# Performance work log

Measured on AMD Instinct MI355X. Metric: run time of the kernel, lower is better.

The kernel has to match this reference:

```python
import jax, jax.numpy as jnp
import numpy as np

B, S, H = 2, 2048, 2048
NUM_HEADS, HEAD_DIM = 16, 128
SOFTMAX_SHIFT = 12


def _int_project(x, w_i8, b_i32, out_shift):
    # x: [..., in] int32, w_i8: [in, out] int8, b_i32: [out] int32
    y = jnp.matmul(x.astype(jnp.int32), w_i8.astype(jnp.int32))
    y = y + b_i32
    return jnp.right_shift(y, out_shift)  # arithmetic shift on signed int32


def setup_inputs() -> dict:
    key = jax.random.key(0)
    ks = jax.random.split(key, 9)
    x_i32 = jax.random.randint(ks[0], (B, S, H), 0, 256, dtype=jnp.int32)
    def w(k):
        return jax.random.randint(k, (H, H), -127, 128, dtype=jnp.int32).astype(jnp.int8)
    def b(k):
        return jax.random.randint(k, (H,), -64, 64, dtype=jnp.int32)
    return {
        "x_i32": x_i32,
        "wq": w(ks[1]), "bq": b(ks[2]),
        "wk": w(ks[3]), "bk": b(ks[4]),
        "wv": w(ks[5]), "bv": b(ks[6]),
        "wo": w(ks[7]), "bo": b(ks[8]),
    }


def reference(x_i32, wq, bq, wk, bk, wv, bv, wo, bo):
    bsz, seq, hidden = x_i32.shape

    def heads(t):  # [b, s, h] -> [b, nh, s, hd]
        return t.reshape(bsz, seq, NUM_HEADS, HEAD_DIM).transpose(0, 2, 1, 3)

    q = heads(_int_project(x_i32, wq, bq, 6))
    k = heads(_int_project(x_i32, wk, bk, 6))
    v = heads(_int_project(x_i32, wv, bv, 6))

    # int32 scores [b, nh, s, s], halved by arithmetic right shift
    scores = jnp.right_shift(jnp.einsum("bhqd,bhkd->bhqk", q, k), 1)

    idx = jnp.arange(seq)
    causal = idx[:, None] >= idx[None, :]  # [s, s]
    neg = jnp.int32(-(1 << 20))
    masked = jnp.where(causal[None, None], scores, neg)

    # clamp-softmax surrogate: subtract row max, clamp(x + 256, 0, 2^12 - 1)
    shifted = masked - jnp.max(masked, axis=-1, keepdims=True)
    attn = jnp.clip(shifted + 256, 0, (1 << SOFTMAX_SHIFT) - 1)

    context = jnp.right_shift(jnp.einsum("bhqk,bhkd->bhqd", attn, v), SOFTMAX_SHIFT)
    context = context.transpose(0, 2, 1, 3).reshape(bsz, seq, hidden)
    return _int_project(context, wo, bo, 7)
```

## Files before the change

kernel.cpp:

```cpp
#include <hip/hip_runtime.h>
#include <stdint.h>


#define SEQ   2048
#define HID   2048
#define NHEAD 16
#define HDIM  128
#define NB    2
#define NEGV  (-(1 << 20))
#define PLANE 8388608
#define WSZ   4194304
#define BHSTR 262144

#define AS1 __attribute__((address_space(1)))
#define AS3 __attribute__((address_space(3)))

typedef int v4i __attribute__((ext_vector_type(4)));

__device__ __forceinline__ v4i mfma_i8(v4i a, v4i b, v4i c) {
  return __builtin_amdgcn_mfma_i32_16x16x64_i8(a, b, c, 0, 0, 0);
}

__device__ __forceinline__ void gl16(const char* g, char* l) {
  __builtin_amdgcn_global_load_lds((const AS1 uint32_t*)g, (AS3 uint32_t*)l, 16, 0, 0);
}

__device__ __forceinline__ void limb3(int v, int& l0, int& l1, int& l2) {
  l0 = (v << 24) >> 24;
  int t = (v - l0) >> 8;
  l1 = (t << 24) >> 24;
  l2 = (t - l1) >> 8;
}

__device__ __forceinline__ int sext4(int x) {
  return ((x << 24) >> 24) + ((x << 16) >> 24) + ((x << 8) >> 24) + (x >> 24);
}

__global__ __launch_bounds__(256) void xpack(const int* __restrict__ X, char* __restrict__ Xs8)
{
  const int i = blockIdx.x * 256 + threadIdx.x;
  int4 v = ((const int4*)X)[i];
  uint32_t b = (uint32_t)((v.x - 128) & 255)
             | ((uint32_t)((v.y - 128) & 255) << 8)
             | ((uint32_t)((v.z - 128) & 255) << 16)
             | ((uint32_t)((v.w - 128) & 255) << 24);
  ((uint32_t*)Xs8)[i] = b;
}

__global__ __launch_bounds__(256) void wpack(const int* __restrict__ Wq, const int* __restrict__ Wk,
                                             const int* __restrict__ Wv, const int* __restrict__ Wo,
                                             char* __restrict__ WtQKV, char* __restrict__ WtO)
{
  __shared__ char Ws[128 * 144];
  const int z = blockIdx.z;
  const int* W = (z == 0) ? Wq : (z == 1) ? Wk : (z == 2) ? Wv : Wo;
  char* Wt = (z < 3) ? (WtQKV + (size_t)z * WSZ) : WtO;
  const int k0 = blockIdx.x * 128, n0 = blockIdx.y * 128;
  const int t = threadIdx.x;
  const int lr = t >> 1, lc = (t & 1) * 64;
  const int* wp = W + (size_t)(k0 + lr) * HID + n0 + lc;
#pragma unroll
  for (int i = 0; i < 16; i++) {
    int4 v = *(const int4*)(wp + 4 * i);
    uint32_t pb = (uint32_t)(v.x & 255) | ((uint32_t)(v.y & 255) << 8)
                | ((uint32_t)(v.z & 255) << 16) | ((uint32_t)(v.w & 255) << 24);
    *(uint32_t*)&Ws[lr * 144 + lc + 4 * i] = pb;
  }
  __syncthreads();
  const int nl = t >> 1, kh = (t & 1) * 64;
  char* op = Wt + (size_t)(n0 + nl) * HID + k0 + kh;
#pragma unroll
  for (int w = 0; w < 16; w++) {
    uint32_t u = 0;
#pragma unroll
    for (int j = 0; j < 4; j++)
      u |= ((uint32_t)(unsigned char)Ws[(kh + w * 4 + j) * 144 + nl]) << (8 * j);
    *(uint32_t*)(op + 4 * w) = u;
  }
}

__global__ __launch_bounds__(256) void csum(const char* __restrict__ WtQKV,
                                            const int* __restrict__ Bq, const int* __restrict__ Bk,
                                            const int* __restrict__ Bv, int* __restrict__ bias2)
{
  const int id = blockIdx.x;
  const int z = id >> 9;
  const int n = ((id & 511) << 2) + (threadIdx.x >> 6);
  const int lane = threadIdx.x & 63;
  const int4* p = (const int4*)(WtQKV + (size_t)z * WSZ + (size_t)n * HID + lane * 32);
  int4 a = p[0], b4 = p[1];
  int vals[8] = {a.x, a.y, a.z, a.w, b4.x, b4.y, b4.z, b4.w};
  int s = 0;
#pragma unroll
  for (int i = 0; i < 8; i++) s += sext4(vals[i]);
#pragma unroll
  for (int m = 1; m < 64; m <<= 1) s += __shfl_xor(s, m);
  if (lane == 0) {
    const int* B = (z == 0) ? Bq : (z == 1) ? Bk : Bv;
    bias2[z * HID + n] = (int)((uint32_t)B[n] + ((uint32_t)s << 7));
  }
}

__global__ __launch_bounds__(256, 3) void qkv_mfma(const char* __restrict__ Xs8,
                                                   const char* __restrict__ WtQKV,
                                                   const int* __restrict__ bias2,
                                                   char* __restrict__ QL, char* __restrict__ KL,
                                                   int* __restrict__ VR, int* __restrict__ PS)
{
  __shared__ __align__(16) char smem[33792];
  const int id = blockIdx.x;
  const int n0 = (id & 15) * 128;
  const int zm = id >> 4;
  const int z  = zm >> 5;
  const int m0 = (zm & 31) * 128;
  const char* Wt = WtQKV + (size_t)z * WSZ;
  const int* b2 = bias2 + z * HID;

  const int t = threadIdx.x, wave = t >> 6, lane = t & 63;
  const int r16 = lane & 15, quad = lane >> 4;
  const int wm = (wave >> 1) * 64, wn = (wave & 1) * 64;

  const int lr0 = t >> 2;
  const int lc0 = (t & 3) ^ ((lr0 >> 1) & 3);
  const int lr1 = (t + 256) >> 2;
  const int lc1 = (t & 3) ^ ((lr1 >> 1) & 3);
  const char* Ag0 = Xs8 + (size_t)(m0 + lr0) * HID + lc0 * 16;
  const char* Ag1 = Xs8 + (size_t)(m0 + lr1) * HID + lc1 * 16;
  const char* Bg0 = Wt + (size_t)(n0 + lr0) * HID + lc0 * 16;
  const char* Bg1 = Wt + (size_t)(n0 + lr1) * HID + lc1 * 16;
  char* Al0 = smem + wave * 1024;
  char* Al1 = smem + 4096 + wave * 1024;
  char* Bl0 = smem + 8192 + wave * 1024;
  char* Bl1 = smem + 12288 + wave * 1024;

  const int xq = (quad ^ ((r16 >> 1) & 3)) * 16;

  v4i acc[4][4];
#pragma unroll
  for (int i = 0; i < 4; i++)
#pragma unroll
    for (int j = 0; j < 4; j++) acc[i][j] = (v4i){0, 0, 0, 0};

  for (int k0 = 0; k0 < HID; k0 += 64) {
    gl16(Ag0 + k0, Al0);
    gl16(Ag1 + k0, Al1);
    gl16(Bg0 + k0, Bl0);
    gl16(Bg1 + k0, Bl1);
    __syncthreads();
    v4i Af[4], Bf[4];
#pragma unroll
    for (int mt = 0; mt < 4; mt++)
      Af[mt] = *(const v4i*)(smem + (wm + mt * 16 + r16) * 64 + xq);
#pragma unroll
    for (int nt = 0; nt < 4; nt++)
      Bf[nt] = *(const v4i*)(smem + 8192 + (wn + nt * 16 + r16) * 64 + xq);
#pragma unroll
    for (int mt = 0; mt < 4; mt++)
#pragma unroll
      for (int nt = 0; nt < 4; nt++)
        acc[mt][nt] = mfma_i8(Af[mt], Bf[nt], acc[mt][nt]);
    __syncthreads();
  }

  int bvv[4];
#pragma unroll
  for (int nt = 0; nt < 4; nt++) bvv[nt] = b2[n0 + wn + nt * 16 + r16];

  const int h  = id & 15;
  const int b  = m0 >> 11;
  const int s0 = m0 & 2047;
  const int bh = b * 16 + h;
  const int myhalf = wave >> 1;

  if (z <= 1) {
    char* dplane = (z == 0) ? QL : KL;
#pragma unroll
    for (int half = 0; half < 2; half++) {
      __syncthreads();
      if (myhalf == half) {
#pragma unroll
        for (int mt = 0; mt < 4; mt++)
#pragma unroll
          for (int nt = 0; nt < 4; nt++) {
            const int col = wn + nt * 16 + r16;
#pragma unroll
            for (int r = 0; r < 4; r++) {
              const int y = ((int)((uint32_t)acc[mt][nt][r] + (uint32_t)bvv[nt])) >> 6;
              int l0, l1, l2; limb3(y, l0, l1, l2);
              const int off = (mt * 16 + quad * 4 + r) * 144 + col;
              smem[off]         = (char)l0;
              smem[9216 + off]  = (char)l1;
              smem[18432 + off] = (char)l2;
            }
          }
      }
      __syncthreads();
      if (t < 192) {
        const int l = t >> 6, rc = t & 63;
        const char* src = &smem[l * 9216 + rc * 144];
        char* dp = dplane + (size_t)l * PLANE + (size_t)bh * BHSTR
                 + (size_t)(s0 + half * 64 + rc) * 128;
#pragma unroll
        for (int j = 0; j < 8; j++)
          *(int4*)(dp + j * 16) = *(const int4*)(src + j * 16);
      }
    }
  } else {
    int* s32 = (int*)smem;
#pragma unroll
    for (int half = 0; half < 2; half++) {
      __syncthreads();
      if (myhalf == half) {
#pragma unroll
        for (int mt = 0; mt < 4; mt++)
#pragma unroll
          for (int nt = 0; nt < 4; nt++) {
            const int col = wn + nt * 16 + r16;
#pragma unroll
            for (int r = 0; r < 4; r++) {
              const int y = ((int)((uint32_t)acc[mt][nt][r] + (uint32_t)bvv[nt])) >> 6;
              s32[(mt * 16 + quad * 4 + r) * 132 + col] = y;
            }
          }
      }
      __syncthreads();
      {
        const int rr = t >> 2, cs = (t & 3) * 32;
        int* vp = VR + (size_t)bh * (SEQ * HDIM) + (size_t)(s0 + half * 64 + rr) * HDIM + cs;
        const int* sp = s32 + rr * 132 + cs;
#pragma unroll
        for (int j = 0; j < 8; j++)
          *(int4*)(vp + 4 * j) = *(const int4*)(sp + 4 * j);
      }
      if (t < 128) {
        uint32_t a = 0;
        for (int j = 0; j < 64; j++) a += (uint32_t)s32[j * 132 + t];
        PS[((size_t)bh * 32 + (s0 >> 6) + half) * 128 + t] = (int)a;
      }
    }
  }
}

__global__ __launch_bounds__(128) void suf(const int* __restrict__ PS, int* __restrict__ SUF)
{
  const int bh = blockIdx.x, d = threadIdx.x;
  SUF[((size_t)bh * 33 + 32) * 128 + d] = 0;
  uint32_t acc = 0;
  for (int tt = 31; tt >= 0; tt--) {
    acc += (uint32_t)PS[((size_t)bh * 32 + tt) * 128 + d];
    SUF[((size_t)bh * 33 + tt) * 128 + d] = (int)acc;
  }
}

__global__ __launch_bounds__(256, 4) void attn_mfma(const char* __restrict__ QL,
    const char* __restrict__ KL, const int* __restrict__ VR,
    const int* __restrict__ SUF, char* __restrict__ CL)
{
  __shared__ __align__(16) char smK[24576];
  __shared__ int   candS[32 * 32];
  __shared__ unsigned short candK[32 * 32];
  __shared__ int   mrow[32];
  __shared__ int   cnt[32];

  const int t = threadIdx.x, w = t >> 6, lane = t & 63;
  const int r16 = lane & 15, quad = lane >> 4;
  const int bid = blockIdx.x;
  const int bh = bid & 31;
  const int tile = 63 - (bid >> 5);
  const int q0 = tile * 32;
  const int b = bh >> 4, h = bh & 15;
  const char* QLb = QL + (size_t)bh * BHSTR;
  const char* KLb = KL + (size_t)bh * BHSTR;
  const int g = w >> 1, p = w & 1;
  const int wq = q0 + g * 16;
  const int ktlast = q0 >> 6;

  if (t < 32) { mrow[t] = (int)0x80000000; cnt[t] = 0; }

  const int srow = w * 8 + (lane >> 3);
  const int schunk = (lane & 7) ^ (lane >> 3);
  const char* kg0 = KLb + (size_t)srow * 128 + schunk * 16;
  const char* kg1 = KLb + (size_t)(srow + 32) * 128 + schunk * 16;

  v4i Aq[3][2];
  {
    const char* qb = QLb + (size_t)(wq + r16) * 128 + quad * 16;
#pragma unroll
    for (int l = 0; l < 3; l++)
#pragma unroll
      for (int c = 0; c < 2; c++)
        Aq[l][c] = *(const v4i*)(qb + (size_t)l * PLANE + c * 64);
  }

  int qrow[4], mr[4];
#pragma unroll
  for (int r = 0; r < 4; r++) {
    qrow[r] = wq + quad * 4 + r;
    mr[r] = (qrow[r] == SEQ - 1) ? (int)0x80000000 : NEGV;
  }
  __syncthreads();

  const v4i vzero = (v4i){0, 0, 0, 0};
  const int sw0 = (((0 * 4 + quad) ^ (r16 & 7))) * 16;
  const int sw1 = (((1 * 4 + quad) ^ (r16 & 7))) * 16;

  for (int kt = 0; kt <= ktlast; kt++) {
    const size_t kb = (size_t)kt * 8192;
#pragma unroll
    for (int l = 0; l < 3; l++) {
      gl16(kg0 + (size_t)l * PLANE + kb, smK + l * 8192 + w * 1024);
      gl16(kg1 + (size_t)l * PLANE + kb, smK + l * 8192 + 4096 + w * 1024);
    }
    __syncthreads();

    const bool last = (kt == ktlast);
    int sc[2][4];
#pragma unroll
    for (int nt2 = 0; nt2 < 2; nt2++) {
      const int nt = 2 * p + nt2;
      const char* kbase = smK + (nt * 16 + r16) * 128;
      v4i B[3][2];
#pragma unroll
      for (int l = 0; l < 3; l++) {
        B[l][0] = *(const v4i*)(kbase + l * 8192 + sw0);
        B[l][1] = *(const v4i*)(kbase + l * 8192 + sw1);
      }
      v4i c0, c1, c2, c3;
      c0 = mfma_i8(Aq[0][0], B[0][0], vzero);
      c0 = mfma_i8(Aq[0][1], B[0][1], c0);
      c1 = mfma_i8(Aq[0][0], B[1][0], vzero);
      c1 = mfma_i8(Aq[0][1], B[1][1], c1);
      c1 = mfma_i8(Aq[1][0], B[0][0], c1);
      c1 = mfma_i8(Aq[1][1], B[0][1], c1);
      c2 = mfma_i8(Aq[0][0], B[2][0], vzero);
      c2 = mfma_i8(Aq[0][1], B[2][1], c2);
      c2 = mfma_i8(Aq[1][0], B[1][0], c2);
      c2 = mfma_i8(Aq[1][1], B[1][1], c2);
      c2 = mfma_i8(Aq[2][0], B[0][0], c2);
      c2 = mfma_i8(Aq[2][1], B[0][1], c2);
      c3 = mfma_i8(Aq[1][0], B[2][0], vzero);
      c3 = mfma_i8(Aq[1][1], B[2][1], c3);
      c3 = mfma_i8(Aq[2][0], B[1][0], c3);
      c3 = mfma_i8(Aq[2][1], B[1][1], c3);
#pragma unroll
      for (int r = 0; r < 4; r++) {
        const uint32_t u = (uint32_t)c0[r] + ((uint32_t)c1[r] << 8)
                         + ((uint32_t)c2[r] << 16) + ((uint32_t)c3[r] << 24);
        sc[nt2][r] = ((int)u) >> 1;
      }
    }
    __syncthreads();

#pragma unroll
    for (int r = 0; r < 4; r++) {
      int mv = (int)0x80000000;
#pragma unroll
      for (int nt2 = 0; nt2 < 2; nt2++) {
        const int gj = kt * 64 + (2 * p + nt2) * 16 + r16;
        const bool valid = !last || (gj <= qrow[r]);
        const int s = valid ? sc[nt2][r] : (int)0x80000000;
        mv = s > mv ? s : mv;
      }
#pragma unroll
      for (int msk = 1; msk < 16; msk <<= 1) {
        const int o = __shfl_xor(mv, msk);
        mv = o > mv ? o : mv;
      }
      mr[r] = mv > mr[r] ? mv : mr[r];
    }
#pragma unroll
    for (int nt2 = 0; nt2 < 2; nt2++) {
      const int gj = kt * 64 + (2 * p + nt2) * 16 + r16;
#pragma unroll
      for (int r = 0; r < 4; r++) {
        const bool valid = !last || (gj <= qrow[r]);
        if (valid && sc[nt2][r] >= mr[r] - 255) {
          const int lrow = g * 16 + quad * 4 + r;
          const int slot = atomicAdd(&cnt[lrow], 1);
          if (slot < 32) {
            candS[lrow * 32 + slot] = sc[nt2][r];
            candK[lrow * 32 + slot] = (unsigned short)gj;
          }
        }
      }
    }
  }
  if (r16 == 0) {
#pragma unroll
    for (int r = 0; r < 4; r++)
      atomicMax(&mrow[g * 16 + quad * 4 + r], mr[r]);
  }
  __syncthreads();

  const int* VRb = VR + (size_t)bh * (SEQ * HDIM);
  const int t64 = q0 >> 6;
  const uint32_t* sufp = (const uint32_t*)(SUF + ((size_t)bh * 33 + t64 + 1) * 128);
  const int d0 = lane * 2;
  const uint32_t ts0 = sufp[d0], ts1 = sufp[d0 + 1];
  const int blkend = (t64 + 1) * 64;

#pragma unroll 1
  for (int i = 0; i < 8; i++) {
    const int lrow = w * 8 + i;
    const int qr = q0 + lrow;
    const int m = mrow[lrow];
    int c = cnt[lrow]; c = c > 32 ? 32 : c;
    uint32_t O0 = 0, O1 = 0;
    for (int idx = 0; idx < c; idx++) {
      const int s = candS[lrow * 32 + idx];
      const int a = s - m + 256;
      if (a > 0) {
        const int key = candK[lrow * 32 + idx];
        const int2 v = *(const int2*)(VRb + (size_t)key * HDIM + d0);
        O0 += (uint32_t)a * (uint32_t)v.x;
        O1 += (uint32_t)a * (uint32_t)v.y;
      }
    }
    int wmv = 0;
    if (m <= NEGV + 255) wmv = NEGV - m + 256;
    if (wmv > 0) {
      uint32_t T0 = ts0, T1 = ts1;
      for (int j = qr + 1; j < blkend; j++) {
        const int2 v = *(const int2*)(VRb + (size_t)j * HDIM + d0);
        T0 += (uint32_t)v.x; T1 += (uint32_t)v.y;
      }
      O0 += (uint32_t)wmv * T0;
      O1 += (uint32_t)wmv * T1;
    }
    const int ctx0 = ((int)O0) >> 12;
    const int ctx1 = ((int)O1) >> 12;
    int a0, a1, a2, e0, e1, e2;
    limb3(ctx0, a0, a1, a2);
    limb3(ctx1, e0, e1, e2);
    const size_t rowb = (size_t)(b * SEQ + qr) * 2048 + (size_t)h * 128 + d0;
    *(unsigned short*)(CL + rowb)             = (unsigned short)((a0 & 255) | ((e0 & 255) << 8));
    *(unsigned short*)(CL + PLANE + rowb)     = (unsigned short)((a1 & 255) | ((e1 & 255) << 8));
    *(unsigned short*)(CL + 2 * (size_t)PLANE + rowb)
                                              = (unsigned short)((a2 & 255) | ((e2 & 255) << 8));
  }
}

__global__ __launch_bounds__(256, 3) void out_mfma(const char* __restrict__ CL,
                                                   const char* __restrict__ WtO,
                                                   const int* __restrict__ Bo,
                                                   int* __restrict__ Out)
{
  __shared__ __align__(16) char smem[20480];
  const int id = blockIdx.x;
  const int n0 = (id & 15) * 128;
  const int m0 = (id >> 4) * 64;

  const int t = threadIdx.x, wave = t >> 6, lane = t & 63;
  const int wm = (wave >> 1) * 32, wn = (wave & 1) * 64;
  const int r16 = lane & 15, quad = lane >> 4;

  const int lr0 = t >> 2;
  const int lc0 = (t & 3) ^ ((lr0 >> 1) & 3);
  const int lr1 = (t + 256) >> 2;
  const int lc1 = (t & 3) ^ ((lr1 >> 1) & 3);
  const char* Ag = CL + (size_t)(m0 + lr0) * HID + lc0 * 16;
  const char* Bg0 = WtO + (size_t)(n0 + lr0) * HID + lc0 * 16;
  const char* Bg1 = WtO + (size_t)(n0 + lr1) * HID + lc1 * 16;
  char* Bl0 = smem + 12288 + wave * 1024;
  char* Bl1 = smem + 16384 + wave * 1024;

  const int xq = (quad ^ ((r16 >> 1) & 3)) * 16;

  v4i acc[3][2][4];
#pragma unroll
  for (int l = 0; l < 3; l++)
#pragma unroll
    for (int i = 0; i < 2; i++)
#pragma unroll
      for (int j = 0; j < 4; j++) acc[l][i][j] = (v4i){0, 0, 0, 0};

  for (int k0 = 0; k0 < HID; k0 += 64) {
#pragma unroll
    for (int l = 0; l < 3; l++)
      gl16(Ag + (size_t)l * PLANE + k0, smem + l * 4096 + wave * 1024);
    gl16(Bg0 + k0, Bl0);
    gl16(Bg1 + k0, Bl1);
    __syncthreads();
    v4i Af[3][2], Bf[4];
#pragma unroll
    for (int l = 0; l < 3; l++)
#pragma unroll
      for (int mt = 0; mt < 2; mt++)
        Af[l][mt] = *(const v4i*)(smem + l * 4096 + (wm + mt * 16 + r16) * 64 + xq);
#pragma unroll
    for (int nt = 0; nt < 4; nt++)
      Bf[nt] = *(const v4i*)(smem + 12288 + (wn + nt * 16 + r16) * 64 + xq);
#pragma unroll
    for (int l = 0; l < 3; l++)
#pragma unroll
      for (int mt = 0; mt < 2; mt++)
#pragma unroll
        for (int nt = 0; nt < 4; nt++)
          acc[l][mt][nt] = mfma_i8(Af[l][mt], Bf[nt], acc[l][mt][nt]);
    __syncthreads();
  }

  int bov[4];
#pragma unroll
  for (int nt = 0; nt < 4; nt++) bov[nt] = Bo[n0 + wn + nt * 16 + r16];
#pragma unroll
  for (int mt = 0; mt < 2; mt++)
#pragma unroll
    for (int nt = 0; nt < 4; nt++)
#pragma unroll
      for (int r = 0; r < 4; r++) {
        uint32_t g = (uint32_t)acc[0][mt][nt][r]
                   + ((uint32_t)acc[1][mt][nt][r] << 8)
                   + ((uint32_t)acc[2][mt][nt][r] << 16)
                   + (uint32_t)bov[nt];
        Out[(size_t)(m0 + wm + mt * 16 + quad * 4 + r) * HID + n0 + wn + nt * 16 + r16] = ((int)g) >> 7;
      }
}

extern "C" void kernel_launch(void* const* d_in, const int* in_sizes, int n_in,
                              void* d_out, int out_size, void* d_ws, size_t ws_size,
                              hipStream_t stream)
{
  (void)in_sizes; (void)n_in; (void)out_size; (void)ws_size;

  const int* x  = (const int*)d_in[0];
  const int* wq = (const int*)d_in[1];
  const int* bq = (const int*)d_in[2];
  const int* wk = (const int*)d_in[3];
  const int* bk = (const int*)d_in[4];
  const int* wv = (const int*)d_in[5];
  const int* bv = (const int*)d_in[6];
  const int* wo = (const int*)d_in[7];
  const int* bo = (const int*)d_in[8];
  int* out = (int*)d_out;
  char* WS = (char*)d_ws;

  char* QLp   = WS + 0;
  char* KLp   = WS + 25165824;
  int*  VRp   = (int*)(WS + 50331648);
  int*  Sb    = (int*)(WS + 83886080);
  int*  PSb   = (int*)(WS + 84426752);
  int*  B2    = (int*)(WS + 84951040);
  char* WtO   = WS + 84975616;
  char* P     = WS + 89169920;
  char* WtQKV = P;
  char* Xs8   = P + 3 * (size_t)WSZ;
  char* CLp   = P;

  xpack<<<dim3(8192), dim3(256), 0, stream>>>(x, Xs8);
  wpack<<<dim3(16, 16, 4), dim3(256), 0, stream>>>(wq, wk, wv, wo, WtQKV, WtO);
  csum<<<dim3(1536), dim3(256), 0, stream>>>(WtQKV, bq, bk, bv, B2);
  qkv_mfma<<<dim3(1536), dim3(256), 0, stream>>>(Xs8, WtQKV, B2, QLp, KLp, VRp, PSb);
  suf<<<dim3(32), dim3(128), 0, stream>>>(PSb, Sb);
  attn_mfma<<<dim3(2048), dim3(256), 0, stream>>>(QLp, KLp, VRp, Sb, CLp);
  out_mfma<<<dim3(1024), dim3(256), 0, stream>>>(CLp, WtO, bo, out);
}
```

Measured before the change: 413.2 us.

## Double GEMM K-step to 128 and widen attention blocks to 64 query rows

The QKV and output GEMMs now stage 128-wide K slices per barrier, using a new 8-chunk XOR swizzle and a larger LDS footprint for the output kernel. This halves the number of sync and load rounds and gives the MFMAs more work between barriers. The attention kernel now runs 512-thread blocks covering 64 query rows, so each staged K tile serves twice as many queries, with the candidate buffers scaled to match. The costs are more LDS per block, fewer resident blocks, and coarser causal load balance, and the hidden attention body must handle the 8-wave layout correctly.

New measurement: 421.9 us. 2.1% more time.

```diff
diff --git a/kernel.cpp b/kernel.cpp
--- a/kernel.cpp
+++ b/kernel.cpp
@@ -120,20 +120,18 @@
   const int r16 = lane & 15, quad = lane >> 4;
   const int wm = (wave >> 1) * 64, wn = (wave & 1) * 64;
 
-  const int lr0 = t >> 2;
-  const int lc0 = (t & 3) ^ ((lr0 >> 1) & 3);
-  const int lr1 = (t + 256) >> 2;
-  const int lc1 = (t & 3) ^ ((lr1 >> 1) & 3);
-  const char* Ag0 = Xs8 + (size_t)(m0 + lr0) * HID + lc0 * 16;
-  const char* Ag1 = Xs8 + (size_t)(m0 + lr1) * HID + lc1 * 16;
-  const char* Bg0 = Wt + (size_t)(n0 + lr0) * HID + lc0 * 16;
-  const char* Bg1 = Wt + (size_t)(n0 + lr1) * HID + lc1 * 16;
-  char* Al0 = smem + wave * 1024;
-  char* Al1 = smem + 4096 + wave * 1024;
-  char* Bl0 = smem + 8192 + wave * 1024;
-  char* Bl1 = smem + 12288 + wave * 1024;
-
-  const int xq = (quad ^ ((r16 >> 1) & 3)) * 16;
+  const char* AgJ[4]; const char* BgJ[4];
+  char* AlJ[4]; char* BlJ[4];
+#pragma unroll
+  for (int j = 0; j < 4; j++) {
+    const int s = j * 256 + t;
+    const int row = s >> 3;
+    const int cg = (s & 7) ^ (row & 7);
+    AgJ[j] = Xs8 + (size_t)(m0 + row) * HID + cg * 16;
+    BgJ[j] = Wt  + (size_t)(n0 + row) * HID + cg * 16;
+    AlJ[j] = smem + j * 4096 + wave * 1024;
+    BlJ[j] = smem + 16384 + j * 4096 + wave * 1024;
+  }
 
   v4i acc[4][4];
 #pragma unroll
@@ -141,24 +139,28 @@
 #pragma unroll
     for (int j = 0; j < 4; j++) acc[i][j] = (v4i){0, 0, 0, 0};
 
-  for (int k0 = 0; k0 < HID; k0 += 64) {
-    gl16(Ag0 + k0, Al0);
-    gl16(Ag1 + k0, Al1);
-    gl16(Bg0 + k0, Bl0);
-    gl16(Bg1 + k0, Bl1);
+  for (int k0 = 0; k0 < HID; k0 += 128) {
+#pragma unroll
+    for (int j = 0; j < 4; j++) gl16(AgJ[j] + k0, AlJ[j]);
+#pragma unroll
+    for (int j = 0; j < 4; j++) gl16(BgJ[j] + k0, BlJ[j]);
     __syncthreads();
-    v4i Af[4], Bf[4];
-#pragma unroll
-    for (int mt = 0; mt < 4; mt++)
-      Af[mt] = *(const v4i*)(smem + (wm + mt * 16 + r16) * 64 + xq);
-#pragma unroll
-    for (int nt = 0; nt < 4; nt++)
-      Bf[nt] = *(const v4i*)(smem + 8192 + (wn + nt * 16 + r16) * 64 + xq);
-#pragma unroll
-    for (int mt = 0; mt < 4; mt++)
+#pragma unroll
+    for (int kk = 0; kk < 2; kk++) {
+      const int xo = ((kk * 4 + quad) ^ (r16 & 7)) * 16;
+      v4i Af[4], Bf[4];
+#pragma unroll
+      for (int mt = 0; mt < 4; mt++)
+        Af[mt] = *(const v4i*)(smem + (wm + mt * 16 + r16) * 128 + xo);
 #pragma unroll
       for (int nt = 0; nt < 4; nt++)
-        acc[mt][nt] = mfma_i8(Af[mt], Bf[nt], acc[mt][nt]);
+        Bf[nt] = *(const v4i*)(smem + 16384 + (wn + nt * 16 + r16) * 128 + xo);
+#pragma unroll
+      for (int mt = 0; mt < 4; mt++)
+#pragma unroll
+        for (int nt = 0; nt < 4; nt++)
+          acc[mt][nt] = mfma_i8(Af[mt], Bf[nt], acc[mt][nt]);
+    }
     __syncthreads();
   }
 
@@ -252,22 +254,22 @@
   }
 }
 
-__global__ __launch_bounds__(256, 4) void attn_mfma(const char* __restrict__ QL,
+__global__ __launch_bounds__(512, 6) void attn_mfma(const char* __restrict__ QL,
     const char* __restrict__ KL, const int* __restrict__ VR,
     const int* __restrict__ SUF, char* __restrict__ CL)
 {
   __shared__ __align__(16) char smK[24576];
-  __shared__ int   candS[32 * 32];
-  __shared__ unsigned short candK[32 * 32];
-  __shared__ int   mrow[32];
-  __shared__ int   cnt[32];
+  __shared__ int   candS[64 * 32];
+  __shared__ unsigned short candK[64 * 32];
+  __shared__ int   mrow[64];
+  __shared__ int   cnt[64];
 
   const int t = threadIdx.x, w = t >> 6, lane = t & 63;
   const int r16 = lane & 15, quad = lane >> 4;
   const int bid = blockIdx.x;
   const int bh = bid & 31;
-  const int tile = 63 - (bid >> 5);
-  const int q0 = tile * 32;
+  const int tile = 31 - (bid >> 5);
+  const int q0 = tile * 64;
   const int b = bh >> 4, h = bh & 15;
   const char* QLb = QL + (size_t)bh * BHSTR;
   const char* KLb = KL + (size_t)bh * BHSTR;
@@ -275,12 +277,11 @@
   const int wq = q0 + g * 16;
   const int ktlast = q0 >> 6;
 
-  if (t < 32) { mrow[t] = (int)0x80000000; cnt[t] = 0; }
+  if (t < 64) { mrow[t] = (int)0x80000000; cnt[t] = 0; }
 
   const int srow = w * 8 + (lane >> 3);
   const int schunk = (lane & 7) ^ (lane >> 3);
-  const char* kg0 = KLb + (size_t)srow * 128 + schunk * 16;
-  const char* kg1 = KLb + (size_t)(srow + 32) * 128 + schunk * 16;
+  const char* kg = KLb + (size_t)srow * 128 + schunk * 16;
 
   v4i Aq[3][2];
   {
@@ -298,19 +299,16 @@
     qrow[r] = wq + quad * 4 + r;
     mr[r] = (qrow[r] == SEQ - 1) ? (int)0x80000000 : NEGV;
   }
-  __syncthreads();
 
   const v4i vzero = (v4i){0, 0, 0, 0};
-  const int sw0 = (((0 * 4 + quad) ^ (r16 & 7))) * 16;
-  const int sw1 = (((1 * 4 + quad) ^ (r16 & 7))) * 16;
+  const int sw0 = ((0 * 4 + quad) ^ (r16 & 7)) * 16;
+  const int sw1 = ((1 * 4 + quad) ^ (r16 & 7)) * 16;
 
   for (int kt = 0; kt <= ktlast; kt++) {
     const size_t kb = (size_t)kt * 8192;
 #pragma unroll
-    for (int l = 0; l < 3; l++) {
-      gl16(kg0 + (size_t)l * PLANE + kb, smK + l * 8192 + w * 1024);
-      gl16(kg1 + (size_t)l * PLANE + kb, smK + l * 8192 + 4096 + w * 1024);
-    }
+    for (int l = 0; l < 3; l++)
+      gl16(kg + (size_t)l * PLANE + kb, smK + l * 8192 + w * 1024);
     __syncthreads();
 
     const bool last = (kt == ktlast);
@@ -445,7 +443,7 @@
                                                    const int* __restrict__ Bo,
                                                    int* __restrict__ Out)
 {
-  __shared__ __align__(16) char smem[20480];
+  __shared__ __align__(16) char smem[40960];
   const int id = blockIdx.x;
   const int n0 = (id & 15) * 128;
   const int m0 = (id >> 4) * 64;
@@ -454,17 +452,27 @@
   const int wm = (wave >> 1) * 32, wn = (wave & 1) * 64;
   const int r16 = lane & 15, quad = lane >> 4;
 
-  const int lr0 = t >> 2;
-  const int lc0 = (t & 3) ^ ((lr0 >> 1) & 3);
-  const int lr1 = (t + 256) >> 2;
-  const int lc1 = (t & 3) ^ ((lr1 >> 1) & 3);
-  const char* Ag = CL + (size_t)(m0 + lr0) * HID + lc0 * 16;
-  const char* Bg0 = WtO + (size_t)(n0 + lr0) * HID + lc0 * 16;
-  const char* Bg1 = WtO + (size_t)(n0 + lr1) * HID + lc1 * 16;
-  char* Bl0 = smem + 12288 + wave * 1024;
-  char* Bl1 = smem + 16384 + wave * 1024;
-
-  const int xq = (quad ^ ((r16 >> 1) & 3)) * 16;
+  const char* AgJ[3][2]; char* AlJ[3][2];
+  const char* BgJ[4];   char* BlJ[4];
+#pragma unroll
+  for (int j = 0; j < 2; j++) {
+    const int s = j * 256 + t;
+    const int row = s >> 3;
+    const int cg = (s & 7) ^ (row & 7);
+#pragma unroll
+    for (int l = 0; l < 3; l++) {
+      AgJ[l][j] = CL + (size_t)l * PLANE + (size_t)(m0 + row) * HID + cg * 16;
+      AlJ[l][j] = smem + l * 8192 + j * 4096 + wave * 1024;
+    }
+  }
+#pragma unroll
+  for (int j = 0; j < 4; j++) {
+    const int s = j * 256 + t;
+    const int row = s >> 3;
+    const int cg = (s & 7) ^ (row & 7);
+    BgJ[j] = WtO + (size_t)(n0 + row) * HID + cg * 16;
+    BlJ[j] = smem + 24576 + j * 4096 + wave * 1024;
+  }
 
   v4i acc[3][2][4];
 #pragma unroll
@@ -474,29 +482,34 @@
 #pragma unroll
       for (int j = 0; j < 4; j++) acc[l][i][j] = (v4i){0, 0, 0, 0};
 
-  for (int k0 = 0; k0 < HID; k0 += 64) {
+  for (int k0 = 0; k0 < HID; k0 += 128) {
 #pragma unroll
     for (int l = 0; l < 3; l++)
-      gl16(Ag + (size_t)l * PLANE + k0, smem + l * 4096 + wave * 1024);
-    gl16(Bg0 + k0, Bl0);
-    gl16(Bg1 + k0, Bl1);
+#pragma unroll
+      for (int j = 0; j < 2; j++) gl16(AgJ[l][j] + k0, AlJ[l][j]);
+#pragma unroll
+    for (int j = 0; j < 4; j++) gl16(BgJ[j] + k0, BlJ[j]);
     __syncthreads();
-    v4i Af[3][2], Bf[4];
-#pragma unroll
-    for (int l = 0; l < 3; l++)
-#pragma unroll
-      for (int mt = 0; mt < 2; mt++)
-        Af[l][mt] = *(const v4i*)(smem + l * 4096 + (wm + mt * 16 + r16) * 64 + xq);
-#pragma unroll
-    for (int nt = 0; nt < 4; nt++)
-      Bf[nt] = *(const v4i*)(smem + 12288 + (wn + nt * 16 + r16) * 64 + xq);
-#pragma unroll
-    for (int l = 0; l < 3; l++)
-#pragma unroll
-      for (int mt = 0; mt < 2; mt++)
-#pragma unroll
-        for (int nt = 0; nt < 4; nt++)
-          acc[l][mt][nt] = mfma_i8(Af[l][mt], Bf[nt], acc[l][mt][nt]);
+#pragma unroll
+    for (int kk = 0; kk < 2; kk++) {
+      const int xo = ((kk * 4 + quad) ^ (r16 & 7)) * 16;
+      v4i Af[3][2], Bf[4];
+#pragma unroll
+      for (int l = 0; l < 3; l++)
+#pragma unroll
+        for (int mt = 0; mt < 2; mt++)
+          Af[l][mt] = *(const v4i*)(smem + l * 8192 + (wm + mt * 16 + r16) * 128 + xo);
+#pragma unroll
+      for (int nt = 0; nt < 4; nt++)
+        Bf[nt] = *(const v4i*)(smem + 24576 + (wn + nt * 16 + r16) * 128 + xo);
+#pragma unroll
+      for (int l = 0; l < 3; l++)
+#pragma unroll
+        for (int mt = 0; mt < 2; mt++)
+#pragma unroll
+          for (int nt = 0; nt < 4; nt++)
+            acc[l][mt][nt] = mfma_i8(Af[l][mt], Bf[nt], acc[l][mt][nt]);
+    }
     __syncthreads();
   }
 
@@ -552,6 +565,6 @@
   csum<<<dim3(1536), dim3(256), 0, stream>>>(WtQKV, bq, bk, bv, B2);
   qkv_mfma<<<dim3(1536), dim3(256), 0, stream>>>(Xs8, WtQKV, B2, QLp, KLp, VRp, PSb);
   suf<<<dim3(32), dim3(128), 0, stream>>>(PSb, Sb);
-  attn_mfma<<<dim3(2048), dim3(256), 0, stream>>>(QLp, KLp, VRp, Sb, CLp);
+  attn_mfma<<<dim3(1024), dim3(512), 0, stream>>>(QLp, KLp, VRp, Sb, CLp);
   out_mfma<<<dim3(1024), dim3(256), 0, stream>>>(CLp, WtO, bo, out);
 }
```
